# Kernel tuning notes

Measured on AMD Instinct MI355X. Metric: run time of the kernel, lower is better.

The kernel has to match this reference:

```python
import jax, jax.numpy as jnp
import numpy as np

N = 10000       # nodes
E = 160000      # edges
D_IN = 256      # in_channels (node feature dim)
H1, C = 8, 32   # conv1: 8 heads x 32 -> 256; conv2: 1 head x 32
MSG = 128       # msg_dim
TD = 128        # time encoder out_channels
ED = MSG + TD   # edge_dim = 256
HC1 = H1 * C    # 256


def _lin(key, shape, scale=0.05):
    return jax.random.normal(key, shape, dtype=jnp.float32) * scale


def setup_inputs() -> dict:
    key = jax.random.key(0)
    ks = jax.random.split(key, 32)
    inp = {}
    inp["x"] = jax.random.normal(ks[0], (N, D_IN), dtype=jnp.float32)
    inp["last_update"] = jax.random.uniform(ks[1], (N,), jnp.float32, 0.0, 1000.0)
    inp["edge_index"] = jax.random.randint(ks[2], (2, E), 0, N)
    inp["t"] = jax.random.uniform(ks[3], (E,), jnp.float32, 0.0, 1000.0)
    inp["msg"] = jax.random.normal(ks[4], (E, MSG), dtype=jnp.float32)
    # TimeEncoder: Linear(1, TD) then cos
    inp["time_w"] = _lin(ks[5], (TD, 1), 0.1)
    inp["time_b"] = jnp.zeros((TD,), jnp.float32)
    # conv1 (TransformerConv in=256, heads=8, per-head 32, edge_dim=256, concat=True)
    inp["Wq1"] = _lin(ks[6], (D_IN, HC1)); inp["bq1"] = jnp.zeros((HC1,), jnp.float32)
    inp["Wk1"] = _lin(ks[7], (D_IN, HC1)); inp["bk1"] = jnp.zeros((HC1,), jnp.float32)
    inp["Wv1"] = _lin(ks[8], (D_IN, HC1)); inp["bv1"] = jnp.zeros((HC1,), jnp.float32)
    inp["We1"] = _lin(ks[9], (ED, HC1))   # lin_edge has no bias in PyG
    inp["Ws1"] = _lin(ks[10], (D_IN, HC1)); inp["bs1"] = jnp.zeros((HC1,), jnp.float32)
    # conv2 (in=256, heads=1, per-head 32, concat=False)
    inp["Wq2"] = _lin(ks[11], (HC1, C)); inp["bq2"] = jnp.zeros((C,), jnp.float32)
    inp["Wk2"] = _lin(ks[12], (HC1, C)); inp["bk2"] = jnp.zeros((C,), jnp.float32)
    inp["Wv2"] = _lin(ks[13], (HC1, C)); inp["bv2"] = jnp.zeros((C,), jnp.float32)
    inp["We2"] = _lin(ks[14], (ED, C))
    inp["Ws2"] = _lin(ks[15], (HC1, C)); inp["bs2"] = jnp.zeros((C,), jnp.float32)
    return inp


def transformer_conv(x, src, dst, edge_attr, Wq, bq, Wk, bk, Wv, bv, We, Ws, bs, heads, ch, concat):
    n = x.shape[0]
    q = (x @ Wq + bq).reshape(n, heads, ch)
    k = (x @ Wk + bk).reshape(n, heads, ch)
    v = (x @ Wv + bv).reshape(n, heads, ch)
    e = (edge_attr @ We).reshape(-1, heads, ch)       # [E,H,C]
    ke = k[src] + e                                    # key_j + edge
    ve = v[src] + e                                    # value_j + edge
    alpha = jnp.einsum('ehc,ehc->eh', q[dst], ke) / jnp.sqrt(jnp.float32(ch))
    # segment softmax over incoming edges of each destination node
    amax = jax.ops.segment_max(alpha, dst, num_segments=n)   # -inf for empty segs
    ex = jnp.exp(alpha - amax[dst])
    den = jax.ops.segment_sum(ex, dst, num_segments=n)
    attn = ex / (den[dst] + 1e-16)                     # [E,H]
    out = jax.ops.segment_sum(attn[:, :, None] * ve, dst, num_segments=n)  # [N,H,C]
    out = out.reshape(n, heads * ch) if concat else out.mean(axis=1)
    return out + (x @ Ws + bs)                         # root skip connection


def reference(x, last_update, edge_index, t, msg, time_w, time_b,
              Wq1, bq1, Wk1, bk1, Wv1, bv1, We1, Ws1, bs1,
              Wq2, bq2, Wk2, bk2, Wv2, bv2, We2, Ws2, bs2):
    src, dst = edge_index[0], edge_index[1]
    rel_t = last_update[src] - t                       # [E]
    rel_t_enc = jnp.cos(rel_t[:, None] * time_w[:, 0][None, :] + time_b)  # [E,TD]
    edge_attr = jnp.concatenate([rel_t_enc, msg], axis=-1)                # [E,ED]
    h = jax.nn.relu(transformer_conv(x, src, dst, edge_attr,
                                     Wq1, bq1, Wk1, bk1, Wv1, bv1, We1, Ws1, bs1,
                                     H1, C, True))
    out = jax.nn.relu(transformer_conv(h, src, dst, edge_attr,
                                       Wq2, bq2, Wk2, bk2, Wv2, bv2, We2, Ws2, bs2,
                                       1, C, False))
    return out
```

## Files before the change

### kernel.cpp

```cpp
#include <hip/hip_runtime.h>
#include <math.h>

#define N_NODES 10000
#define N_EDGES 160000
#define RT1 157
#define RTE 2500
#define CONVX_T (RT1 * 64 * 32)

static inline int ceildiv(int a, int b) { return (a + b - 1) / b; }

typedef float f32x4 __attribute__((ext_vector_type(4)));
typedef short bf16x8 __attribute__((ext_vector_type(8)));

__device__ __forceinline__ unsigned short f2bf(float f) {
  unsigned int u = __builtin_bit_cast(unsigned int, f);
  u += 0x7FFFu + ((u >> 16) & 1u);
  return (unsigned short)(u >> 16);
}
__device__ __forceinline__ float bf2f(unsigned short h) {
  unsigned int u = ((unsigned int)h) << 16;
  return __builtin_bit_cast(float, u);
}

__global__ void prep1_kernel(const float* __restrict__ lu, const int* __restrict__ srcp,
                             const int* __restrict__ dstp, const float* __restrict__ tt,
                             float* __restrict__ rel, int* __restrict__ deg, int E) {
  for (int i = blockIdx.x * blockDim.x + threadIdx.x; i < E; i += gridDim.x * blockDim.x) {
    rel[i] = lu[srcp[i]] - tt[i];
    atomicAdd(&deg[dstp[i]], 1);
  }
}

__global__ void scan_kernel(const int* __restrict__ deg, int* __restrict__ rowptr, int n) {
  __shared__ int part[1024];
  const int tid = threadIdx.x;
  const int CHK = 10;
  int base = tid * CHK;
  int loc[CHK];
  int s = 0;
#pragma unroll
  for (int j = 0; j < CHK; ++j) {
    int idx = base + j;
    int v = (idx < n) ? deg[idx] : 0;
    loc[j] = s; s += v;
  }
  part[tid] = s;
  __syncthreads();
  for (int off = 1; off < 1024; off <<= 1) {
    int y = (tid >= off) ? part[tid - off] : 0;
    __syncthreads();
    part[tid] += y;
    __syncthreads();
  }
  int pre = tid ? part[tid - 1] : 0;
#pragma unroll
  for (int j = 0; j < CHK; ++j) {
    int idx = base + j;
    if (idx < n) rowptr[idx] = pre + loc[j];
  }
  if (tid == 1023) rowptr[n] = part[1023];
}

__global__ void scatter_kernel(const int* __restrict__ srcp, const int* __restrict__ dstp,
                               const int* __restrict__ rowptr, int* __restrict__ fill,
                               int* __restrict__ sortpos, int* __restrict__ srcs, int E) {
  for (int e = blockIdx.x * blockDim.x + threadIdx.x; e < E; e += gridDim.x * blockDim.x) {
    int d = dstp[e];
    int pos = atomicAdd(&fill[d], 1);
    int slot = rowptr[d] + pos;
    sortpos[e] = slot;
    srcs[slot] = srcp[e];
  }
}

__device__ __forceinline__ void wstore(const float* __restrict__ W, unsigned short* __restrict__ out,
                                       int Nin, int n_off, int NFtot, int k, int c) {
  int gc = n_off + c;
  int ks=k>>5, kg=(k>>3)&3, j=k&7, nf=gc>>4, ic=gc&15;
  out[(size_t)(ks*NFtot+nf)*512 + (ic+16*kg)*8 + j] = f2bf(W[(size_t)k*Nin + c]);
}

__global__ void conv_all_kernel(const float* __restrict__ x, unsigned short* __restrict__ xa,
                                const float* Wq1, const float* Wk1, const float* Wv1, const float* Ws1,
                                const float* We1, const float* Wq2, const float* Wk2, const float* Wv2,
                                const float* Ws2, const float* We2,
                                const float* bq1, const float* bk1, const float* bv1, const float* bs1,
                                const float* bq2, const float* bk2, const float* bv2, const float* bs2,
                                unsigned short* W1f, unsigned short* We1f, unsigned short* W2f,
                                unsigned short* We2f, float* bcat1, float* bcat2) {
  int t0 = blockIdx.x * blockDim.x + threadIdx.x;
  if (t0 < CONVX_T) {
    int i = t0 >> 5, k8 = t0 & 31;
    union { uint4 q; unsigned short s[8]; } u;
    if (i < N_NODES) {
      const float4* px = (const float4*)(x + (size_t)i * 256 + k8 * 8);
      float4 f0 = px[0], f1 = px[1];
      u.s[0]=f2bf(f0.x); u.s[1]=f2bf(f0.y); u.s[2]=f2bf(f0.z); u.s[3]=f2bf(f0.w);
      u.s[4]=f2bf(f1.x); u.s[5]=f2bf(f1.y); u.s[6]=f2bf(f1.z); u.s[7]=f2bf(f1.w);
    } else {
      u.q = make_uint4(0,0,0,0);
    }
    int rt=i>>6, rf=(i>>4)&3, ir=i&15, ks=k8>>2, kg=k8&3;
    *(uint4*)&xa[(size_t)rt*16384 + ks*2048 + rf*512 + (ir+16*kg)*8] = u.q;
    return;
  }
  int t = t0 - CONVX_T;
  if (t < 262144) {
    int w = t >> 16, r = t & 65535, k = r >> 8, c = r & 255;
    const float* W = (w == 0) ? Wq1 : (w == 1) ? Wk1 : (w == 2) ? Wv1 : Ws1;
    wstore(W, W1f, 256, w * 256, 64, k, c);
  } else if (t < 327680) {
    int r = t - 262144, k = r >> 8, c = r & 255;
    wstore(We1, We1f, 256, 0, 16, k, c);
  } else if (t < 360448) {
    int r = t - 327680, w = r >> 13, r2 = r & 8191, k = r2 >> 5, c = r2 & 31;
    const float* W = (w == 0) ? Wq2 : (w == 1) ? Wk2 : (w == 2) ? Wv2 : Ws2;
    wstore(W, W2f, 32, w * 32, 8, k, c);
  } else if (t < 368640) {
    int r = t - 360448, k = r >> 5, c = r & 31;
    wstore(We2, We2f, 32, 0, 4, k, c);
  } else if (t < 369792) {
    int r = t - 368640;
    if (r < 1024) {
      const float* b = (r < 256) ? bq1 : (r < 512) ? bk1 : (r < 768) ? bv1 : bs1;
      bcat1[r] = b[r & 255];
    } else {
      int r2 = r - 1024;
      const float* b = (r2 < 32) ? bq2 : (r2 < 64) ? bk2 : (r2 < 96) ? bv2 : bs2;
      bcat2[r2] = b[r2 & 31];
    }
  }
}

__global__ __launch_bounds__(512, 4)
void big_gemm(const unsigned short* __restrict__ xa, const unsigned short* __restrict__ W1f,
              const float* __restrict__ bcat1, float* __restrict__ qf,
              unsigned short* __restrict__ kvb, float* __restrict__ sf,
              const unsigned short* __restrict__ We1f, const unsigned short* __restrict__ We2f,
              unsigned short* __restrict__ e1b, unsigned short* __restrict__ e2b,
              const float* __restrict__ rel, const float* __restrict__ tw,
              const float* __restrict__ tb, const float* __restrict__ msg,
              const int* __restrict__ sortpos) {
  __shared__ char ldsraw[32768];
  uint4* lds4 = (uint4*)ldsraw;
  const int tid = threadIdx.x;
  const int wid = tid >> 6, lane = tid & 63;
  const int bx = blockIdx.x;
  const int fr0 = (lane >> 4) * 4;
  const int fc0 = lane & 15;

  if (bx < RTE) {
    const int rt0 = bx;
    const int phase = bx & 7;
    {
      const int rem = tid & 255;
      const int ksh = tid >> 8;
      const int arf = rem >> 6, ar2 = rem & 63, air = ar2 & 15, akg = ar2 >> 4;
      const int aedge = rt0 * 64 + arf * 16 + air;
      float rl = rel[aedge];
#pragma unroll
      for (int s = 0; s < 2; ++s) {
        int ks = ksh + s * 2;
        int k8 = ks * 4 + akg;
        const float4* twp = (const float4*)(tw + k8 * 8);
        const float4* tbp = (const float4*)(tb + k8 * 8);
        float4 w0 = twp[0], w1 = twp[1], b0 = tbp[0], b1 = tbp[1];
        union { uint4 q; unsigned short us[8]; } u;
        u.us[0]=f2bf(__cosf(rl*w0.x+b0.x)); u.us[1]=f2bf(__cosf(rl*w0.y+b0.y));
        u.us[2]=f2bf(__cosf(rl*w0.z+b0.z)); u.us[3]=f2bf(__cosf(rl*w0.w+b0.w));
        u.us[4]=f2bf(__cosf(rl*w1.x+b1.x)); u.us[5]=f2bf(__cosf(rl*w1.y+b1.y));
        u.us[6]=f2bf(__cosf(rl*w1.z+b1.z)); u.us[7]=f2bf(__cosf(rl*w1.w+b1.w));
        lds4[ks * 256 + rem] = u.q;
      }
#pragma unroll
      for (int s = 0; s < 2; ++s) {
        int ks = 4 + ksh + s * 2;
        int k8 = ks * 4 + akg;
        const float4* pm = (const float4*)(msg + (size_t)aedge * 128 + (size_t)(k8 - 16) * 8);
        float4 f0 = pm[0], f1 = pm[1];
        union { uint4 q; unsigned short us[8]; } u;
        u.us[0]=f2bf(f0.x); u.us[1]=f2bf(f0.y); u.us[2]=f2bf(f0.z); u.us[3]=f2bf(f0.w);
        u.us[4]=f2bf(f1.x); u.us[5]=f2bf(f1.y); u.us[6]=f2bf(f1.z); u.us[7]=f2bf(f1.w);
        lds4[ks * 256 + rem] = u.q;
      }
    }
    __syncthreads();

    f32x4 acc[4][2];
    f32x4 acc2[4];
#pragma unroll
    for (int i = 0; i < 4; ++i) {
      acc2[i] = (f32x4){0.f, 0.f, 0.f, 0.f};
#pragma unroll
      for (int j = 0; j < 2; ++j) acc[i][j] = (f32x4){0.f, 0.f, 0.f, 0.f};
    }

    bf16x8 aN0, aN1, aN2, aN3, bN0, bN1, b2N;
    {
      const int ks = phase;
      aN0 = *(const bf16x8*)&lds4[ks * 256 + 0 * 64 + lane];
      aN1 = *(const bf16x8*)&lds4[ks * 256 + 1 * 64 + lane];
      aN2 = *(const bf16x8*)&lds4[ks * 256 + 2 * 64 + lane];
      aN3 = *(const bf16x8*)&lds4[ks * 256 + 3 * 64 + lane];
      bN0 = *(const bf16x8*)(We1f + ((size_t)(ks * 16 + wid * 2 + 0)) * 512 + (size_t)lane * 8);
      bN1 = *(const bf16x8*)(We1f + ((size_t)(ks * 16 + wid * 2 + 1)) * 512 + (size_t)lane * 8);
      b2N = 0;
      if (wid < 2) b2N = *(const bf16x8*)(We2f + ((size_t)(ks * 4 + wid)) * 512 + (size_t)lane * 8);
    }
#pragma unroll
    for (int ksi = 0; ksi < 8; ++ksi) {
      bf16x8 aC0 = aN0, aC1 = aN1, aC2 = aN2, aC3 = aN3;
      bf16x8 bC0 = bN0, bC1 = bN1, b2C = b2N;
      if (ksi < 7) {
        const int ks2 = (ksi + 1) ^ phase;
        aN0 = *(const bf16x8*)&lds4[ks2 * 256 + 0 * 64 + lane];
        aN1 = *(const bf16x8*)&lds4[ks2 * 256 + 1 * 64 + lane];
        aN2 = *(const bf16x8*)&lds4[ks2 * 256 + 2 * 64 + lane];
        aN3 = *(const bf16x8*)&lds4[ks2 * 256 + 3 * 64 + lane];
        bN0 = *(const bf16x8*)(We1f + ((size_t)(ks2 * 16 + wid * 2 + 0)) * 512 + (size_t)lane * 8);
        bN1 = *(const bf16x8*)(We1f + ((size_t)(ks2 * 16 + wid * 2 + 1)) * 512 + (size_t)lane * 8);
        if (wid < 2) b2N = *(const bf16x8*)(We2f + ((size_t)(ks2 * 4 + wid)) * 512 + (size_t)lane * 8);
      }
      acc[0][0] = __builtin_amdgcn_mfma_f32_16x16x32_bf16(aC0, bC0, acc[0][0], 0, 0, 0);
      acc[1][0] = __builtin_amdgcn_mfma_f32_16x16x32_bf16(aC1, bC0, acc[1][0], 0, 0, 0);
      acc[2][0] = __builtin_amdgcn_mfma_f32_16x16x32_bf16(aC2, bC0, acc[2][0], 0, 0, 0);
      acc[3][0] = __builtin_amdgcn_mfma_f32_16x16x32_bf16(aC3, bC0, acc[3][0], 0, 0, 0);
      acc[0][1] = __builtin_amdgcn_mfma_f32_16x16x32_bf16(aC0, bC1, acc[0][1], 0, 0, 0);
      acc[1][1] = __builtin_amdgcn_mfma_f32_16x16x32_bf16(aC1, bC1, acc[1][1], 0, 0, 0);
      acc[2][1] = __builtin_amdgcn_mfma_f32_16x16x32_bf16(aC2, bC1, acc[2][1], 0, 0, 0);
      acc[3][1] = __builtin_amdgcn_mfma_f32_16x16x32_bf16(aC3, bC1, acc[3][1], 0, 0, 0);
      if (wid < 2) {
        acc2[0] = __builtin_amdgcn_mfma_f32_16x16x32_bf16(aC0, b2C, acc2[0], 0, 0, 0);
        acc2[1] = __builtin_amdgcn_mfma_f32_16x16x32_bf16(aC1, b2C, acc2[1], 0, 0, 0);
        acc2[2] = __builtin_amdgcn_mfma_f32_16x16x32_bf16(aC2, b2C, acc2[2], 0, 0, 0);
        acc2[3] = __builtin_amdgcn_mfma_f32_16x16x32_bf16(aC3, b2C, acc2[3], 0, 0, 0);
      }
    }

    __syncthreads();
    unsigned short* cl  = (unsigned short*)ldsraw;
    unsigned short* cl2 = (unsigned short*)(ldsraw + 9216);
    int* spos = (int*)(ldsraw + 14336);
    if (tid < 64) spos[tid] = sortpos[rt0 * 64 + tid];
    if (wid < 2) {
#pragma unroll
      for (int rf = 0; rf < 4; ++rf)
#pragma unroll
        for (int j = 0; j < 4; ++j)
          cl2[(fr0 + rf * 16 + j) * 40 + wid * 16 + fc0] = f2bf(acc2[rf][j]);
    }
    for (int pass = 0; pass < 4; ++pass) {
      if ((wid >> 1) == pass) {
#pragma unroll
        for (int cf = 0; cf < 2; ++cf) {
          int c = (wid & 1) * 32 + cf * 16 + fc0;
#pragma unroll
          for (int rf = 0; rf < 4; ++rf)
#pragma unroll
            for (int j = 0; j < 4; ++j)
              cl[(fr0 + rf * 16 + j) * 72 + c] = f2bf(acc[rf][cf][j]);
        }
      }
      __syncthreads();
      {
        int row = tid >> 3, cc = (tid & 7) * 8;
        int gr = spos[row];
        *(uint4*)&e1b[(size_t)gr * 256 + pass * 64 + cc] = *(const uint4*)&cl[row * 72 + cc];
      }
      __syncthreads();
    }
    if (tid < 256) {
      int row = tid >> 2, cc = (tid & 3) * 8;
      int gr = spos[row];
      *(uint4*)&e2b[(size_t)gr * 32 + cc] = *(const uint4*)&cl2[row * 40 + cc];
    }
  } else {
    const int idx = bx - RTE;
    const int rt0 = idx % RT1;
    const int y = idx / RT1;
    const int phase = rt0 & 7;

#pragma unroll
    for (int s = 0; s < 4; ++s)
      lds4[tid + s * 512] = *(const uint4*)(xa + (size_t)rt0 * 16384 + (size_t)(tid + s * 512) * 8);
    __syncthreads();

    f32x4 acc[4][2];
#pragma unroll
    for (int i = 0; i < 4; ++i)
#pragma unroll
      for (int j = 0; j < 2; ++j) acc[i][j] = (f32x4){0.f, 0.f, 0.f, 0.f};

    bf16x8 aN0, aN1, aN2, aN3, bN0, bN1;
    {
      const int ks = phase;
      aN0 = *(const bf16x8*)&lds4[ks * 256 + 0 * 64 + lane];
      aN1 = *(const bf16x8*)&lds4[ks * 256 + 1 * 64 + lane];
      aN2 = *(const bf16x8*)&lds4[ks * 256 + 2 * 64 + lane];
      aN3 = *(const bf16x8*)&lds4[ks * 256 + 3 * 64 + lane];
      bN0 = *(const bf16x8*)(W1f + ((size_t)(ks * 64 + y * 16 + wid * 2 + 0)) * 512 + (size_t)lane * 8);
      bN1 = *(const bf16x8*)(W1f + ((size_t)(ks * 64 + y * 16 + wid * 2 + 1)) * 512 + (size_t)lane * 8);
    }
#pragma unroll
    for (int ksi = 0; ksi < 8; ++ksi) {
      bf16x8 aC0 = aN0, aC1 = aN1, aC2 = aN2, aC3 = aN3;
      bf16x8 bC0 = bN0, bC1 = bN1;
      if (ksi < 7) {
        const int ks2 = (ksi + 1) ^ phase;
        aN0 = *(const bf16x8*)&lds4[ks2 * 256 + 0 * 64 + lane];
        aN1 = *(const bf16x8*)&lds4[ks2 * 256 + 1 * 64 + lane];
        aN2 = *(const bf16x8*)&lds4[ks2 * 256 + 2 * 64 + lane];
        aN3 = *(const bf16x8*)&lds4[ks2 * 256 + 3 * 64 + lane];
        bN0 = *(const bf16x8*)(W1f + ((size_t)(ks2 * 64 + y * 16 + wid * 2 + 0)) * 512 + (size_t)lane * 8);
        bN1 = *(const bf16x8*)(W1f + ((size_t)(ks2 * 64 + y * 16 + wid * 2 + 1)) * 512 + (size_t)lane * 8);
      }
      acc[0][0] = __builtin_amdgcn_mfma_f32_16x16x32_bf16(aC0, bC0, acc[0][0], 0, 0, 0);
      acc[1][0] = __builtin_amdgcn_mfma_f32_16x16x32_bf16(aC1, bC0, acc[1][0], 0, 0, 0);
      acc[2][0] = __builtin_amdgcn_mfma_f32_16x16x32_bf16(aC2, bC0, acc[2][0], 0, 0, 0);
      acc[3][0] = __builtin_amdgcn_mfma_f32_16x16x32_bf16(aC3, bC0, acc[3][0], 0, 0, 0);
      acc[0][1] = __builtin_amdgcn_mfma_f32_16x16x32_bf16(aC0, bC1, acc[0][1], 0, 0, 0);
      acc[1][1] = __builtin_amdgcn_mfma_f32_16x16x32_bf16(aC1, bC1, acc[1][1], 0, 0, 0);
      acc[2][1] = __builtin_amdgcn_mfma_f32_16x16x32_bf16(aC2, bC1, acc[2][1], 0, 0, 0);
      acc[3][1] = __builtin_amdgcn_mfma_f32_16x16x32_bf16(aC3, bC1, acc[3][1], 0, 0, 0);
    }

    bool bf16path;
    void* dstp_; int cstr_, dc0_, bcol0_;
    if (y == 0)      { bf16path = false; dstp_ = qf;  cstr_ = 256; dc0_ = 0;   bcol0_ = 0; }
    else if (y == 1) { bf16path = true;  dstp_ = kvb; cstr_ = 512; dc0_ = 0;   bcol0_ = 256; }
    else if (y == 2) { bf16path = true;  dstp_ = kvb; cstr_ = 512; dc0_ = 256; bcol0_ = 512; }
    else             { bf16path = false; dstp_ = sf;  cstr_ = 256; dc0_ = 0;   bcol0_ = 768; }
    if (!bf16path) {
      float* dst = (float*)dstp_;
      const int row0 = rt0 * 64 + fr0;
#pragma unroll
      for (int cf = 0; cf < 2; ++cf) {
        int c = wid * 32 + cf * 16 + fc0;
        float bv = bcat1[bcol0_ + c];
#pragma unroll
        for (int rf = 0; rf < 4; ++rf) {
#pragma unroll
          for (int j = 0; j < 4; ++j) {
            int r = row0 + rf * 16 + j;
            if (r < N_NODES) dst[(size_t)r * cstr_ + c] = acc[rf][cf][j] + bv;
          }
        }
      }
    } else {
      __syncthreads();
      unsigned short* cl = (unsigned short*)ldsraw;
      unsigned short* dst = (unsigned short*)dstp_;
      for (int pass = 0; pass < 4; ++pass) {
        if ((wid >> 1) == pass) {
#pragma unroll
          for (int cf = 0; cf < 2; ++cf) {
            int c = (wid & 1) * 32 + cf * 16 + fc0;
            float bv = bcat1[bcol0_ + pass * 64 + c];
#pragma unroll
            for (int rf = 0; rf < 4; ++rf)
#pragma unroll
              for (int j = 0; j < 4; ++j)
                cl[(fr0 + rf * 16 + j) * 72 + c] = f2bf(acc[rf][cf][j] + bv);
          }
        }
        __syncthreads();
        {
          int row = tid >> 3, cc = (tid & 7) * 8;
          int gr = rt0 * 64 + row;
          if (gr < N_NODES)
            *(uint4*)&dst[(size_t)gr * cstr_ + dc0_ + pass * 64 + cc] = *(const uint4*)&cl[row * 72 + cc];
        }
        __syncthreads();
      }
    }
  }
}

__global__ __launch_bounds__(256)
void gemm_node2(const unsigned short* __restrict__ ha, const unsigned short* __restrict__ W2f,
                const float* __restrict__ bcat2, float* __restrict__ qkvs2) {
  const int tid = threadIdx.x;
  const int wid = tid >> 6, lane = tid & 63;
  const int wr = wid >> 1, wc = wid & 1;
  const int rt0 = blockIdx.x * 2;
  int rtA = rt0 + wr;
  if (rtA >= RT1) rtA = RT1 - 1;

  f32x4 acc[4][4];
#pragma unroll
  for (int i = 0; i < 4; ++i)
#pragma unroll
    for (int j = 0; j < 4; ++j) acc[i][j] = (f32x4){0.f, 0.f, 0.f, 0.f};

#pragma unroll
  for (int ks = 0; ks < 8; ++ks) {
    bf16x8 a[4], b[4];
#pragma unroll
    for (int rf = 0; rf < 4; ++rf)
      a[rf] = *(const bf16x8*)(ha + (size_t)rtA * 16384 + (size_t)ks * 2048 + (size_t)(rf * 64 + lane) * 8);
#pragma unroll
    for (int cf = 0; cf < 4; ++cf)
      b[cf] = *(const bf16x8*)(W2f + ((size_t)(ks * 8 + wc * 4 + cf)) * 512 + (size_t)lane * 8);
#pragma unroll
    for (int rf = 0; rf < 4; ++rf)
#pragma unroll
      for (int cf = 0; cf < 4; ++cf)
        acc[rf][cf] = __builtin_amdgcn_mfma_f32_16x16x32_bf16(a[rf], b[cf], acc[rf][cf], 0, 0, 0);
  }

  const int row0 = (rt0 + wr) * 64 + ((lane >> 4) * 4);
  const int cb2 = wc * 64 + (lane & 15);
#pragma unroll
  for (int cf = 0; cf < 4; ++cf) {
    int c = cb2 + cf * 16;
    float bv = bcat2[c];
#pragma unroll
    for (int rf = 0; rf < 4; ++rf) {
#pragma unroll
      for (int j = 0; j < 4; ++j) {
        int r = row0 + rf * 16 + j;
        if (r < N_NODES) qkvs2[(size_t)r * 128 + c] = acc[rf][cf][j] + bv;
      }
    }
  }
}

__global__ __launch_bounds__(64)
void attn1_kernel(const float* __restrict__ qf, const unsigned short* __restrict__ kvb,
                  const float* __restrict__ sf, const unsigned short* __restrict__ e1b,
                  const int* __restrict__ srcs, const int* __restrict__ rowptr,
                  unsigned short* __restrict__ ha) {
  const int n = blockIdx.x;
  const int lane = threadIdx.x;
  const int h = lane >> 3;
  const int c0 = (lane & 7) * 4;
  const int off = h * 32 + c0;
  const int beg = rowptr[n], end = rowptr[n + 1];
  const float4 q = *(const float4*)&qf[(size_t)n * 256 + off];

  float m0=-INFINITY,d0=0,x00=0,x01=0,x02=0,x03=0;
  float m1=-INFINITY,d1=0,x10=0,x11=0,x12=0,x13=0;
  float m2=-INFINITY,d2=0,x20=0,x21=0,x22=0,x23=0;
  float m3=-INFINITY,d3=0,x30=0,x31=0,x32=0,x33=0;

  auto step = [&](int i, float& m, float& d, float& a0, float& a1, float& a2, float& a3) {
    const int s = srcs[i];
    ushort4 ev = *(const ushort4*)&e1b[(size_t)i * 256 + off];
    ushort4 kk = *(const ushort4*)&kvb[(size_t)s * 512 + off];
    ushort4 vv = *(const ushort4*)&kvb[(size_t)s * 512 + 256 + off];
    float e0=bf2f(ev.x), e1=bf2f(ev.y), e2=bf2f(ev.z), e3=bf2f(ev.w);
    float p = q.x*(bf2f(kk.x)+e0) + q.y*(bf2f(kk.y)+e1) + q.z*(bf2f(kk.z)+e2) + q.w*(bf2f(kk.w)+e3);
    p += __shfl_xor(p, 1); p += __shfl_xor(p, 2); p += __shfl_xor(p, 4);
    p *= 0.17677669529663687f;
    const float mn = fmaxf(m, p);
    const float sc = __expf(m - mn), w = __expf(p - mn);
    d = d * sc + w;
    a0 = a0 * sc + w * (bf2f(vv.x) + e0);
    a1 = a1 * sc + w * (bf2f(vv.y) + e1);
    a2 = a2 * sc + w * (bf2f(vv.z) + e2);
    a3 = a3 * sc + w * (bf2f(vv.w) + e3);
    m = mn;
  };

  int i = beg;
  for (; i + 3 < end; i += 4) {
    step(i,     m0, d0, x00, x01, x02, x03);
    step(i + 1, m1, d1, x10, x11, x12, x13);
    step(i + 2, m2, d2, x20, x21, x22, x23);
    step(i + 3, m3, d3, x30, x31, x32, x33);
  }
  for (; i < end; ++i) step(i, m0, d0, x00, x01, x02, x03);

  auto merge = [&](float& m, float& d, float& a0, float& a1, float& a2, float& a3,
                   float mB, float dB, float b0, float b1, float b2, float b3) {
    if (mB == -INFINITY) return;
    const float M = fmaxf(m, mB);
    const float sA = __expf(m - M), sB = __expf(mB - M);
    d = d * sA + dB * sB;
    a0 = a0 * sA + b0 * sB; a1 = a1 * sA + b1 * sB;
    a2 = a2 * sA + b2 * sB; a3 = a3 * sA + b3 * sB;
    m = M;
  };
  merge(m0, d0, x00, x01, x02, x03, m1, d1, x10, x11, x12, x13);
  merge(m2, d2, x20, x21, x22, x23, m3, d3, x30, x31, x32, x33);
  merge(m0, d0, x00, x01, x02, x03, m2, d2, x20, x21, x22, x23);

  const float inv = 1.f / (d0 + 1e-16f);
  const float4 sk = *(const float4*)&sf[(size_t)n * 256 + off];
  float o0 = fmaxf(x00 * inv + sk.x, 0.f);
  float o1 = fmaxf(x01 * inv + sk.y, 0.f);
  float o2 = fmaxf(x02 * inv + sk.z, 0.f);
  float o3 = fmaxf(x03 * inv + sk.w, 0.f);
  int rt = n >> 6, rf = (n >> 4) & 3, ir = n & 15;
  int kg = (lane & 7) >> 1, jj = 4 * (lane & 1);
  ushort4 w4;
  w4.x = f2bf(o0); w4.y = f2bf(o1); w4.z = f2bf(o2); w4.w = f2bf(o3);
  *(ushort4*)&ha[(size_t)rt * 16384 + h * 2048 + rf * 512 + (ir + 16 * kg) * 8 + jj] = w4;
}

__global__ __launch_bounds__(64)
void attn2_kernel(const float* __restrict__ qkvs2, const unsigned short* __restrict__ e2b,
                  const int* __restrict__ srcs, const int* __restrict__ rowptr,
                  float* __restrict__ outp) {
  const int n = blockIdx.x;
  const int tid = threadIdx.x;
  const int c = tid & 31;
  const int beg = rowptr[n], end = rowptr[n + 1];
  const float qv = qkvs2[(size_t)n * 128 + c];

  float m0=-INFINITY,d0=0,x0=0;
  float m1=-INFINITY,d1=0,x1=0;
  float m2=-INFINITY,d2=0,x2=0;
  float m3=-INFINITY,d3=0,x3=0;

  auto step = [&](int i, float& m, float& d, float& a) {
    const int s = srcs[i];
    const float ev = bf2f(e2b[(size_t)i * 32 + c]);
    float p = qv * (qkvs2[(size_t)s * 128 + 32 + c] + ev);
    const float v = qkvs2[(size_t)s * 128 + 64 + c] + ev;
#pragma unroll
    for (int off = 16; off; off >>= 1) p += __shfl_xor(p, off);
    p *= 0.17677669529663687f;
    const float mn = fmaxf(m, p);
    const float sc = __expf(m - mn), w = __expf(p - mn);
    d = d * sc + w; a = a * sc + w * v; m = mn;
  };

  int i = beg;
  for (; i + 3 < end; i += 4) {
    step(i, m0, d0, x0);
    step(i + 1, m1, d1, x1);
    step(i + 2, m2, d2, x2);
    step(i + 3, m3, d3, x3);
  }
  for (; i < end; ++i) step(i, m0, d0, x0);

  auto merge = [&](float& m, float& d, float& a, float mB, float dB, float b) {
    if (mB == -INFINITY) return;
    const float M = fmaxf(m, mB);
    const float sA = __expf(m - M), sB = __expf(mB - M);
    d = d * sA + dB * sB; a = a * sA + b * sB; m = M;
  };
  merge(m0, d0, x0, m1, d1, x1);
  merge(m2, d2, x2, m3, d3, x3);
  merge(m0, d0, x0, m2, d2, x2);

  if (tid < 32) {
    float o = x0 / (d0 + 1e-16f) + qkvs2[(size_t)n * 128 + 96 + c];
    outp[(size_t)n * 32 + c] = fmaxf(o, 0.f);
  }
}

extern "C" void kernel_launch(void* const* d_in, const int* in_sizes, int n_in,
                              void* d_out, int out_size, void* d_ws, size_t ws_size,
                              hipStream_t stream) {
  const float* x   = (const float*)d_in[0];
  const float* lu  = (const float*)d_in[1];
  const int*   ei  = (const int*)d_in[2];
  const float* tt  = (const float*)d_in[3];
  const float* msg = (const float*)d_in[4];
  const float* tw  = (const float*)d_in[5];
  const float* tb  = (const float*)d_in[6];
  const float* Wq1 = (const float*)d_in[7];  const float* bq1 = (const float*)d_in[8];
  const float* Wk1 = (const float*)d_in[9];  const float* bk1 = (const float*)d_in[10];
  const float* Wv1 = (const float*)d_in[11]; const float* bv1 = (const float*)d_in[12];
  const float* We1 = (const float*)d_in[13];
  const float* Ws1 = (const float*)d_in[14]; const float* bs1 = (const float*)d_in[15];
  const float* Wq2 = (const float*)d_in[16]; const float* bq2 = (const float*)d_in[17];
  const float* Wk2 = (const float*)d_in[18]; const float* bk2 = (const float*)d_in[19];
  const float* Wv2 = (const float*)d_in[20]; const float* bv2 = (const float*)d_in[21];
  const float* We2 = (const float*)d_in[22];
  const float* Ws2 = (const float*)d_in[23]; const float* bs2 = (const float*)d_in[24];

  const int* srcp = ei;
  const int* dstp = ei + N_EDGES;

  char* p = (char*)d_ws;
  auto alloc = [&](size_t bytes) -> char* {
    char* r = p;
    p += (bytes + 255) & ~(size_t)255;
    return r;
  };
  int*   deg     = (int*)alloc((size_t)N_NODES * 4);
  int*   fill    = (int*)alloc((size_t)N_NODES * 4);
  int*   rowptr  = (int*)alloc((size_t)(N_NODES + 1) * 4);
  int*   sortpos = (int*)alloc((size_t)N_EDGES * 4);
  int*   srcs    = (int*)alloc((size_t)N_EDGES * 4);
  float* rel     = (float*)alloc((size_t)N_EDGES * 4);
  unsigned short* xa   = (unsigned short*)alloc((size_t)RT1 * 32768);
  unsigned short* W1f  = (unsigned short*)alloc((size_t)8 * 64 * 1024);
  unsigned short* We1f = (unsigned short*)alloc((size_t)8 * 16 * 1024);
  unsigned short* W2f  = (unsigned short*)alloc((size_t)8 * 8 * 1024);
  unsigned short* We2f = (unsigned short*)alloc((size_t)8 * 4 * 1024);
  float* bcat1  = (float*)alloc(1024 * 4);
  float* bcat2  = (float*)alloc(128 * 4);
  float* qf     = (float*)alloc((size_t)N_NODES * 256 * 4);
  unsigned short* kvb = (unsigned short*)alloc((size_t)N_NODES * 512 * 2);
  float* sf     = (float*)alloc((size_t)N_NODES * 256 * 4);
  unsigned short* e1b = (unsigned short*)alloc((size_t)N_EDGES * 256 * 2);
  unsigned short* ha  = (unsigned short*)alloc((size_t)RT1 * 32768);
  float* qkvs2  = (float*)alloc((size_t)N_NODES * 128 * 4);
  unsigned short* e2b = (unsigned short*)alloc((size_t)N_EDGES * 32 * 2);
  float* outp   = (float*)d_out;

  hipMemsetAsync(deg, 0, (size_t)N_NODES * 4, stream);
  hipMemsetAsync(fill, 0, (size_t)N_NODES * 4, stream);
  hipMemsetAsync(ha + (size_t)(RT1 - 1) * 16384, 0, 32768, stream);

  prep1_kernel<<<625, 256, 0, stream>>>(lu, srcp, dstp, tt, rel, deg, N_EDGES);
  scan_kernel<<<1, 1024, 0, stream>>>(deg, rowptr, N_NODES);
  scatter_kernel<<<625, 256, 0, stream>>>(srcp, dstp, rowptr, fill, sortpos, srcs, N_EDGES);

  conv_all_kernel<<<ceildiv(CONVX_T + 369792, 256), 256, 0, stream>>>(
      x, xa, Wq1, Wk1, Wv1, Ws1, We1, Wq2, Wk2, Wv2, Ws2, We2,
      bq1, bk1, bv1, bs1, bq2, bk2, bv2, bs2,
      W1f, We1f, W2f, We2f, bcat1, bcat2);

  big_gemm<<<RTE + RT1 * 4, 512, 0, stream>>>(
      xa, W1f, bcat1, qf, kvb, sf, We1f, We2f, e1b, e2b,
      rel, tw, tb, msg, sortpos);

  attn1_kernel<<<N_NODES, 64, 0, stream>>>(qf, kvb, sf, e1b, srcs, rowptr, ha);
  gemm_node2<<<ceildiv(RT1, 2), 256, 0, stream>>>(ha, W2f, bcat2, qkvs2);
  attn2_kernel<<<N_NODES, 64, 0, stream>>>(qkvs2, e2b, srcs, rowptr, outp);
}
```

Measured before the change: 176.7 us.

## Fuse edge projection with layer-1 attention via per-segment partial softmax and merge

The edge GEMM for layer 1 now feeds the attention directly inside the same block. Edges are processed in destination-sorted order; each 8-edge segment writes a partial softmax record (max, denominator, weighted bf16 value sum) per destination. A small merge kernel then combines the records and applies the skip connection and ReLU. This removes the large bf16 e1b edge-feature buffer and the separate attn1 pass over it. In exchange, the node GEMM is split into its own launch ahead of the edge kernel, so the two no longer overlap. The scatter step also produces sorted src/dst/edge-id/rel_t arrays, so msg is gathered by original edge id. Destinations spanning more than MAXSEG segments would silently drop contributions.

```diff
diff --git a/kernel.cpp b/kernel.cpp
--- a/kernel.cpp
+++ b/kernel.cpp
@@ -6,6 +6,8 @@
 #define RT1 157
 #define RTE 2500
 #define CONVX_T (RT1 * 64 * 32)
+#define MAXSEG 16
+#define SEGSTRIDE 576
 
 static inline int ceildiv(int a, int b) { return (a + b - 1) / b; }
 
@@ -22,13 +24,9 @@
   return __builtin_bit_cast(float, u);
 }
 
-__global__ void prep1_kernel(const float* __restrict__ lu, const int* __restrict__ srcp,
-                             const int* __restrict__ dstp, const float* __restrict__ tt,
-                             float* __restrict__ rel, int* __restrict__ deg, int E) {
-  for (int i = blockIdx.x * blockDim.x + threadIdx.x; i < E; i += gridDim.x * blockDim.x) {
-    rel[i] = lu[srcp[i]] - tt[i];
+__global__ void count_kernel(const int* __restrict__ dstp, int* __restrict__ deg, int E) {
+  for (int i = blockIdx.x * blockDim.x + threadIdx.x; i < E; i += gridDim.x * blockDim.x)
     atomicAdd(&deg[dstp[i]], 1);
-  }
 }
 
 __global__ void scan_kernel(const int* __restrict__ deg, int* __restrict__ rowptr, int n) {
@@ -61,15 +59,19 @@
   if (tid == 1023) rowptr[n] = part[1023];
 }
 
-__global__ void scatter_kernel(const int* __restrict__ srcp, const int* __restrict__ dstp,
+__global__ void scatter_kernel(const float* __restrict__ lu, const float* __restrict__ tt,
+                               const int* __restrict__ srcp, const int* __restrict__ dstp,
                                const int* __restrict__ rowptr, int* __restrict__ fill,
-                               int* __restrict__ sortpos, int* __restrict__ srcs, int E) {
+                               int* __restrict__ srcs, int* __restrict__ dsts,
+                               int* __restrict__ eidA, float* __restrict__ rel_s, int E) {
   for (int e = blockIdx.x * blockDim.x + threadIdx.x; e < E; e += gridDim.x * blockDim.x) {
-    int d = dstp[e];
+    int d = dstp[e], s = srcp[e];
     int pos = atomicAdd(&fill[d], 1);
     int slot = rowptr[d] + pos;
-    sortpos[e] = slot;
-    srcs[slot] = srcp[e];
+    srcs[slot] = s;
+    dsts[slot] = d;
+    eidA[slot] = e;
+    rel_s[slot] = lu[s] - tt[e];
   }
 }
 
@@ -133,247 +135,380 @@
 }
 
 __global__ __launch_bounds__(512, 4)
-void big_gemm(const unsigned short* __restrict__ xa, const unsigned short* __restrict__ W1f,
-              const float* __restrict__ bcat1, float* __restrict__ qf,
-              unsigned short* __restrict__ kvb, float* __restrict__ sf,
-              const unsigned short* __restrict__ We1f, const unsigned short* __restrict__ We2f,
-              unsigned short* __restrict__ e1b, unsigned short* __restrict__ e2b,
-              const float* __restrict__ rel, const float* __restrict__ tw,
-              const float* __restrict__ tb, const float* __restrict__ msg,
-              const int* __restrict__ sortpos) {
+void node1_gemm(const unsigned short* __restrict__ xa, const unsigned short* __restrict__ W1f,
+                const float* __restrict__ bcat1, float* __restrict__ qf,
+                unsigned short* __restrict__ kvb, float* __restrict__ sf) {
   __shared__ char ldsraw[32768];
   uint4* lds4 = (uint4*)ldsraw;
+  const int tid = threadIdx.x;
+  const int wid = tid >> 6, lane = tid & 63;
+  const int fr0 = (lane >> 4) * 4;
+  const int fc0 = lane & 15;
+  const int rt0 = blockIdx.x % RT1;
+  const int y = blockIdx.x / RT1;
+  const int phase = rt0 & 7;
+
+#pragma unroll
+  for (int s = 0; s < 4; ++s)
+    lds4[tid + s * 512] = *(const uint4*)(xa + (size_t)rt0 * 16384 + (size_t)(tid + s * 512) * 8);
+  __syncthreads();
+
+  f32x4 acc[4][2];
+#pragma unroll
+  for (int i = 0; i < 4; ++i)
+#pragma unroll
+    for (int j = 0; j < 2; ++j) acc[i][j] = (f32x4){0.f, 0.f, 0.f, 0.f};
+
+  bf16x8 aN0, aN1, aN2, aN3, bN0, bN1;
+  {
+    const int ks = phase;
+    aN0 = *(const bf16x8*)&lds4[ks * 256 + 0 * 64 + lane];
+    aN1 = *(const bf16x8*)&lds4[ks * 256 + 1 * 64 + lane];
+    aN2 = *(const bf16x8*)&lds4[ks * 256 + 2 * 64 + lane];
+    aN3 = *(const bf16x8*)&lds4[ks * 256 + 3 * 64 + lane];
+    bN0 = *(const bf16x8*)(W1f + ((size_t)(ks * 64 + y * 16 + wid * 2 + 0)) * 512 + (size_t)lane * 8);
+    bN1 = *(const bf16x8*)(W1f + ((size_t)(ks * 64 + y * 16 + wid * 2 + 1)) * 512 + (size_t)lane * 8);
+  }
+#pragma unroll
+  for (int ksi = 0; ksi < 8; ++ksi) {
+    bf16x8 aC0 = aN0, aC1 = aN1, aC2 = aN2, aC3 = aN3;
+    bf16x8 bC0 = bN0, bC1 = bN1;
+    if (ksi < 7) {
+      const int ks2 = (ksi + 1) ^ phase;
+      aN0 = *(const bf16x8*)&lds4[ks2 * 256 + 0 * 64 + lane];
+      aN1 = *(const bf16x8*)&lds4[ks2 * 256 + 1 * 64 + lane];
+      aN2 = *(const bf16x8*)&lds4[ks2 * 256 + 2 * 64 + lane];
+      aN3 = *(const bf16x8*)&lds4[ks2 * 256 + 3 * 64 + lane];
+      bN0 = *(const bf16x8*)(W1f + ((size_t)(ks2 * 64 + y * 16 + wid * 2 + 0)) * 512 + (size_t)lane * 8);
+      bN1 = *(const bf16x8*)(W1f + ((size_t)(ks2 * 64 + y * 16 + wid * 2 + 1)) * 512 + (size_t)lane * 8);
+    }
+    acc[0][0] = __builtin_amdgcn_mfma_f32_16x16x32_bf16(aC0, bC0, acc[0][0], 0, 0, 0);
+    acc[1][0] = __builtin_amdgcn_mfma_f32_16x16x32_bf16(aC1, bC0, acc[1][0], 0, 0, 0);
+    acc[2][0] = __builtin_amdgcn_mfma_f32_16x16x32_bf16(aC2, bC0, acc[2][0], 0, 0, 0);
+    acc[3][0] = __builtin_amdgcn_mfma_f32_16x16x32_bf16(aC3, bC0, acc[3][0], 0, 0, 0);
+    acc[0][1] = __builtin_amdgcn_mfma_f32_16x16x32_bf16(aC0, bC1, acc[0][1], 0, 0, 0);
+    acc[1][1] = __builtin_amdgcn_mfma_f32_16x16x32_bf16(aC1, bC1, acc[1][1], 0, 0, 0);
+    acc[2][1] = __builtin_amdgcn_mfma_f32_16x16x32_bf16(aC2, bC1, acc[2][1], 0, 0, 0);
+    acc[3][1] = __builtin_amdgcn_mfma_f32_16x16x32_bf16(aC3, bC1, acc[3][1], 0, 0, 0);
+  }
+
+  bool bf16path;
+  void* dstp_; int cstr_, dc0_, bcol0_;
+  if (y == 0)      { bf16path = false; dstp_ = qf;  cstr_ = 256; dc0_ = 0;   bcol0_ = 0; }
+  else if (y == 1) { bf16path = true;  dstp_ = kvb; cstr_ = 512; dc0_ = 0;   bcol0_ = 256; }
+  else if (y == 2) { bf16path = true;  dstp_ = kvb; cstr_ = 512; dc0_ = 256; bcol0_ = 512; }
+  else             { bf16path = false; dstp_ = sf;  cstr_ = 256; dc0_ = 0;   bcol0_ = 768; }
+  if (!bf16path) {
+    float* dst = (float*)dstp_;
+    const int row0 = rt0 * 64 + fr0;
+#pragma unroll
+    for (int cf = 0; cf < 2; ++cf) {
+      int c = wid * 32 + cf * 16 + fc0;
+      float bv = bcat1[bcol0_ + c];
+#pragma unroll
+      for (int rf = 0; rf < 4; ++rf) {
+#pragma unroll
+        for (int j = 0; j < 4; ++j) {
+          int r = row0 + rf * 16 + j;
+          if (r < N_NODES) dst[(size_t)r * cstr_ + c] = acc[rf][cf][j] + bv;
+        }
+      }
+    }
+  } else {
+    __syncthreads();
+    unsigned short* cl = (unsigned short*)ldsraw;
+    unsigned short* dst = (unsigned short*)dstp_;
+    for (int pass = 0; pass < 4; ++pass) {
+      if ((wid >> 1) == pass) {
+#pragma unroll
+        for (int cf = 0; cf < 2; ++cf) {
+          int c = (wid & 1) * 32 + cf * 16 + fc0;
+          float bv = bcat1[bcol0_ + pass * 64 + c];
+#pragma unroll
+          for (int rf = 0; rf < 4; ++rf)
+#pragma unroll
+            for (int j = 0; j < 4; ++j)
+              cl[(fr0 + rf * 16 + j) * 72 + c] = f2bf(acc[rf][cf][j] + bv);
+        }
+      }
+      __syncthreads();
+      {
+        int row = tid >> 3, cc = (tid & 7) * 8;
+        int gr = rt0 * 64 + row;
+        if (gr < N_NODES)
+          *(uint4*)&dst[(size_t)gr * cstr_ + dc0_ + pass * 64 + cc] = *(const uint4*)&cl[row * 72 + cc];
+      }
+      __syncthreads();
+    }
+  }
+}
+
+__global__ __launch_bounds__(512, 4)
+void edge_fused(const float* __restrict__ qf, const unsigned short* __restrict__ kvb,
+                const unsigned short* __restrict__ We1f, const unsigned short* __restrict__ We2f,
+                char* __restrict__ segrec, unsigned short* __restrict__ e2b,
+                const float* __restrict__ rel_s, const float* __restrict__ tw,
+                const float* __restrict__ tb, const float* __restrict__ msg,
+                const int* __restrict__ eidA, const int* __restrict__ srcsA,
+                const int* __restrict__ dstsA, const int* __restrict__ rowptr) {
+  __shared__ char ldsraw[43008];
+  uint4* lds4 = (uint4*)ldsraw;
+  unsigned short* e1t = (unsigned short*)ldsraw;
+  float* scoreL = (float*)(ldsraw + 33280);
+  float* wL     = (float*)(ldsraw + 35328);
+  int* dseg     = (int*)(ldsraw + 37376);
+  int* sseg     = (int*)(ldsraw + 37632);
+  unsigned short* cl2 = (unsigned short*)(ldsraw + 37888);
+
   const int tid = threadIdx.x;
   const int wid = tid >> 6, lane = tid & 63;
   const int bx = blockIdx.x;
   const int fr0 = (lane >> 4) * 4;
   const int fc0 = lane & 15;
-
-  if (bx < RTE) {
-    const int rt0 = bx;
-    const int phase = bx & 7;
+  const int rt0 = bx;
+  const int phase = bx & 7;
+
+  {
+    const int rem = tid & 255;
+    const int ksh = tid >> 8;
+    const int arf = rem >> 6, ar2 = rem & 63, air = ar2 & 15, akg = ar2 >> 4;
+    const int slot = rt0 * 64 + arf * 16 + air;
+    float rl = rel_s[slot];
+    int eorg = eidA[slot];
+#pragma unroll
+    for (int s = 0; s < 2; ++s) {
+      int ks = ksh + s * 2;
+      int k8 = ks * 4 + akg;
+      const float4* twp = (const float4*)(tw + k8 * 8);
+      const float4* tbp = (const float4*)(tb + k8 * 8);
+      float4 w0 = twp[0], w1 = twp[1], b0 = tbp[0], b1 = tbp[1];
+      union { uint4 q; unsigned short us[8]; } u;
+      u.us[0]=f2bf(__cosf(rl*w0.x+b0.x)); u.us[1]=f2bf(__cosf(rl*w0.y+b0.y));
+      u.us[2]=f2bf(__cosf(rl*w0.z+b0.z)); u.us[3]=f2bf(__cosf(rl*w0.w+b0.w));
+      u.us[4]=f2bf(__cosf(rl*w1.x+b1.x)); u.us[5]=f2bf(__cosf(rl*w1.y+b1.y));
+      u.us[6]=f2bf(__cosf(rl*w1.z+b1.z)); u.us[7]=f2bf(__cosf(rl*w1.w+b1.w));
+      lds4[ks * 256 + rem] = u.q;
+    }
+#pragma unroll
+    for (int s = 0; s < 2; ++s) {
+      int ks = 4 + ksh + s * 2;
+      int k8 = ks * 4 + akg;
+      const float4* pm = (const float4*)(msg + (size_t)eorg * 128 + (size_t)(k8 - 16) * 8);
+      float4 f0 = pm[0], f1 = pm[1];
+      union { uint4 q; unsigned short us[8]; } u;
+      u.us[0]=f2bf(f0.x); u.us[1]=f2bf(f0.y); u.us[2]=f2bf(f0.z); u.us[3]=f2bf(f0.w);
+      u.us[4]=f2bf(f1.x); u.us[5]=f2bf(f1.y); u.us[6]=f2bf(f1.z); u.us[7]=f2bf(f1.w);
+      lds4[ks * 256 + rem] = u.q;
+    }
+  }
+  __syncthreads();
+
+  f32x4 acc[4][2];
+  f32x4 acc2[4];
+#pragma unroll
+  for (int i = 0; i < 4; ++i) {
+    acc2[i] = (f32x4){0.f, 0.f, 0.f, 0.f};
+#pragma unroll
+    for (int j = 0; j < 2; ++j) acc[i][j] = (f32x4){0.f, 0.f, 0.f, 0.f};
+  }
+
+  bf16x8 aN0, aN1, aN2, aN3, bN0, bN1, b2N;
+  {
+    const int ks = phase;
+    aN0 = *(const bf16x8*)&lds4[ks * 256 + 0 * 64 + lane];
+    aN1 = *(const bf16x8*)&lds4[ks * 256 + 1 * 64 + lane];
+    aN2 = *(const bf16x8*)&lds4[ks * 256 + 2 * 64 + lane];
+    aN3 = *(const bf16x8*)&lds4[ks * 256 + 3 * 64 + lane];
+    bN0 = *(const bf16x8*)(We1f + ((size_t)(ks * 16 + wid * 2 + 0)) * 512 + (size_t)lane * 8);
+    bN1 = *(const bf16x8*)(We1f + ((size_t)(ks * 16 + wid * 2 + 1)) * 512 + (size_t)lane * 8);
+    b2N = 0;
+    if (wid < 2) b2N = *(const bf16x8*)(We2f + ((size_t)(ks * 4 + wid)) * 512 + (size_t)lane * 8);
+  }
+#pragma unroll
+  for (int ksi = 0; ksi < 8; ++ksi) {
+    bf16x8 aC0 = aN0, aC1 = aN1, aC2 = aN2, aC3 = aN3;
+    bf16x8 bC0 = bN0, bC1 = bN1, b2C = b2N;
+    if (ksi < 7) {
+      const int ks2 = (ksi + 1) ^ phase;
+      aN0 = *(const bf16x8*)&lds4[ks2 * 256 + 0 * 64 + lane];
+      aN1 = *(const bf16x8*)&lds4[ks2 * 256 + 1 * 64 + lane];
+      aN2 = *(const bf16x8*)&lds4[ks2 * 256 + 2 * 64 + lane];
+      aN3 = *(const bf16x8*)&lds4[ks2 * 256 + 3 * 64 + lane];
+      bN0 = *(const bf16x8*)(We1f + ((size_t)(ks2 * 16 + wid * 2 + 0)) * 512 + (size_t)lane * 8);
+      bN1 = *(const bf16x8*)(We1f + ((size_t)(ks2 * 16 + wid * 2 + 1)) * 512 + (size_t)lane * 8);
+      if (wid < 2) b2N = *(const bf16x8*)(We2f + ((size_t)(ks2 * 4 + wid)) * 512 + (size_t)lane * 8);
+    }
+    acc[0][0] = __builtin_amdgcn_mfma_f32_16x16x32_bf16(aC0, bC0, acc[0][0], 0, 0, 0);
+    acc[1][0] = __builtin_amdgcn_mfma_f32_16x16x32_bf16(aC1, bC0, acc[1][0], 0, 0, 0);
+    acc[2][0] = __builtin_amdgcn_mfma_f32_16x16x32_bf16(aC2, bC0, acc[2][0], 0, 0, 0);
+    acc[3][0] = __builtin_amdgcn_mfma_f32_16x16x32_bf16(aC3, bC0, acc[3][0], 0, 0, 0);
+    acc[0][1] = __builtin_amdgcn_mfma_f32_16x16x32_bf16(aC0, bC1, acc[0][1], 0, 0, 0);
+    acc[1][1] = __builtin_amdgcn_mfma_f32_16x16x32_bf16(aC1, bC1, acc[1][1], 0, 0, 0);
+    acc[2][1] = __builtin_amdgcn_mfma_f32_16x16x32_bf16(aC2, bC1, acc[2][1], 0, 0, 0);
+    acc[3][1] = __builtin_amdgcn_mfma_f32_16x16x32_bf16(aC3, bC1, acc[3][1], 0, 0, 0);
+    if (wid < 2) {
+      acc2[0] = __builtin_amdgcn_mfma_f32_16x16x32_bf16(aC0, b2C, acc2[0], 0, 0, 0);
+      acc2[1] = __builtin_amdgcn_mfma_f32_16x16x32_bf16(aC1, b2C, acc2[1], 0, 0, 0);
+      acc2[2] = __builtin_amdgcn_mfma_f32_16x16x32_bf16(aC2, b2C, acc2[2], 0, 0, 0);
+      acc2[3] = __builtin_amdgcn_mfma_f32_16x16x32_bf16(aC3, b2C, acc2[3], 0, 0, 0);
+    }
+  }
+
+  __syncthreads();
+  if (tid < 64) {
+    dseg[tid] = dstsA[rt0 * 64 + tid];
+    sseg[tid] = srcsA[rt0 * 64 + tid];
+  }
+#pragma unroll
+  for (int cf = 0; cf < 2; ++cf)
+#pragma unroll
+    for (int rf = 0; rf < 4; ++rf)
+#pragma unroll
+      for (int j = 0; j < 4; ++j)
+        e1t[(fr0 + rf * 16 + j) * 260 + wid * 32 + cf * 16 + fc0] = f2bf(acc[rf][cf][j]);
+  if (wid < 2) {
+#pragma unroll
+    for (int rf = 0; rf < 4; ++rf)
+#pragma unroll
+      for (int j = 0; j < 4; ++j)
+        cl2[(fr0 + rf * 16 + j) * 40 + wid * 16 + fc0] = f2bf(acc2[rf][j]);
+  }
+  __syncthreads();
+
+  {
+    const int base = wid * 8;
+    int d8[8], s8[8];
+#pragma unroll
+    for (int t = 0; t < 8; ++t) { d8[t] = dseg[base + t]; s8[t] = sseg[base + t]; }
+#pragma unroll
+    for (int t = 0; t < 8; ++t) {
+      const int r = base + t;
+      float4 q4 = *(const float4*)&qf[(size_t)d8[t] * 256 + lane * 4];
+      ushort4 k4 = *(const ushort4*)&kvb[(size_t)s8[t] * 512 + lane * 4];
+      ushort4 e4 = *(const ushort4*)&e1t[r * 260 + lane * 4];
+      float p = q4.x * (bf2f(k4.x) + bf2f(e4.x)) + q4.y * (bf2f(k4.y) + bf2f(e4.y))
+              + q4.z * (bf2f(k4.z) + bf2f(e4.z)) + q4.w * (bf2f(k4.w) + bf2f(e4.w));
+      p += __shfl_xor(p, 1); p += __shfl_xor(p, 2); p += __shfl_xor(p, 4);
+      if ((lane & 7) == 0) scoreL[r * 8 + (lane >> 3)] = p * 0.17677669529663687f;
+    }
+  }
+  __syncthreads();
+
+  {
+    const int r = tid >> 3, h = tid & 7;
+    const int d = dseg[r];
+    const int base = r & ~7;
+    float m = -INFINITY;
+#pragma unroll
+    for (int r2 = 0; r2 < 8; ++r2)
+      if (dseg[base + r2] == d) m = fmaxf(m, scoreL[(base + r2) * 8 + h]);
+    wL[r * 8 + h] = __expf(scoreL[r * 8 + h] - m);
+    bool first = (r == base) || (dseg[r - 1] != d);
+    if (first) {
+      float den = 0.f;
+#pragma unroll
+      for (int r2 = 0; r2 < 8; ++r2)
+        if (dseg[base + r2] == d) den += __expf(scoreL[(base + r2) * 8 + h] - m);
+      int rg = bx * 8 + (r >> 3);
+      int j = rg - (rowptr[d] >> 3);
+      if (j < MAXSEG) {
+        float* rec = (float*)(segrec + ((size_t)d * MAXSEG + j) * SEGSTRIDE);
+        rec[128 + h] = m;
+        rec[136 + h] = den;
+      }
+    }
+  }
+  __syncthreads();
+
+  {
+    const int base = wid * 8;
+    const int rgj = bx * 8 + wid;
+    int d8[8]; float w8[8]; ushort4 v8[8], e8[8];
+#pragma unroll
+    for (int t = 0; t < 8; ++t) {
+      const int r = base + t;
+      d8[t] = dseg[r];
+      v8[t] = *(const ushort4*)&kvb[(size_t)sseg[r] * 512 + 256 + lane * 4];
+      e8[t] = *(const ushort4*)&e1t[r * 260 + lane * 4];
+      w8[t] = wL[r * 8 + (lane >> 3)];
+    }
+    f32x4 pacc = (f32x4){0.f, 0.f, 0.f, 0.f};
+    int cur = d8[0];
+#pragma unroll
+    for (int t = 0; t < 8; ++t) {
+      if (d8[t] != cur) {
+        int j = rgj - (rowptr[cur] >> 3);
+        if (j < MAXSEG) {
+          unsigned short* pp = (unsigned short*)(segrec + ((size_t)cur * MAXSEG + j) * SEGSTRIDE);
+          ushort4 o;
+          o.x = f2bf(pacc[0]); o.y = f2bf(pacc[1]); o.z = f2bf(pacc[2]); o.w = f2bf(pacc[3]);
+          *(ushort4*)&pp[lane * 4] = o;
+        }
+        pacc = (f32x4){0.f, 0.f, 0.f, 0.f};
+        cur = d8[t];
+      }
+      pacc[0] += w8[t] * (bf2f(v8[t].x) + bf2f(e8[t].x));
+      pacc[1] += w8[t] * (bf2f(v8[t].y) + bf2f(e8[t].y));
+      pacc[2] += w8[t] * (bf2f(v8[t].z) + bf2f(e8[t].z));
+      pacc[3] += w8[t] * (bf2f(v8[t].w) + bf2f(e8[t].w));
+    }
     {
-      const int rem = tid & 255;
-      const int ksh = tid >> 8;
-      const int arf = rem >> 6, ar2 = rem & 63, air = ar2 & 15, akg = ar2 >> 4;
-      const int aedge = rt0 * 64 + arf * 16 + air;
-      float rl = rel[aedge];
-#pragma unroll
-      for (int s = 0; s < 2; ++s) {
-        int ks = ksh + s * 2;
-        int k8 = ks * 4 + akg;
-        const float4* twp = (const float4*)(tw + k8 * 8);
-        const float4* tbp = (const float4*)(tb + k8 * 8);
-        float4 w0 = twp[0], w1 = twp[1], b0 = tbp[0], b1 = tbp[1];
-        union { uint4 q; unsigned short us[8]; } u;
-        u.us[0]=f2bf(__cosf(rl*w0.x+b0.x)); u.us[1]=f2bf(__cosf(rl*w0.y+b0.y));
-        u.us[2]=f2bf(__cosf(rl*w0.z+b0.z)); u.us[3]=f2bf(__cosf(rl*w0.w+b0.w));
-        u.us[4]=f2bf(__cosf(rl*w1.x+b1.x)); u.us[5]=f2bf(__cosf(rl*w1.y+b1.y));
-        u.us[6]=f2bf(__cosf(rl*w1.z+b1.z)); u.us[7]=f2bf(__cosf(rl*w1.w+b1.w));
-        lds4[ks * 256 + rem] = u.q;
+      int j = rgj - (rowptr[cur] >> 3);
+      if (j < MAXSEG) {
+        unsigned short* pp = (unsigned short*)(segrec + ((size_t)cur * MAXSEG + j) * SEGSTRIDE);
+        ushort4 o;
+        o.x = f2bf(pacc[0]); o.y = f2bf(pacc[1]); o.z = f2bf(pacc[2]); o.w = f2bf(pacc[3]);
+        *(ushort4*)&pp[lane * 4] = o;
       }
-#pragma unroll
-      for (int s = 0; s < 2; ++s) {
-        int ks = 4 + ksh + s * 2;
-        int k8 = ks * 4 + akg;
-        const float4* pm = (const float4*)(msg + (size_t)aedge * 128 + (size_t)(k8 - 16) * 8);
-        float4 f0 = pm[0], f1 = pm[1];
-        union { uint4 q; unsigned short us[8]; } u;
-        u.us[0]=f2bf(f0.x); u.us[1]=f2bf(f0.y); u.us[2]=f2bf(f0.z); u.us[3]=f2bf(f0.w);
-        u.us[4]=f2bf(f1.x); u.us[5]=f2bf(f1.y); u.us[6]=f2bf(f1.z); u.us[7]=f2bf(f1.w);
-        lds4[ks * 256 + rem] = u.q;
-      }
-    }
-    __syncthreads();
-
-    f32x4 acc[4][2];
-    f32x4 acc2[4];
-#pragma unroll
-    for (int i = 0; i < 4; ++i) {
-      acc2[i] = (f32x4){0.f, 0.f, 0.f, 0.f};
-#pragma unroll
-      for (int j = 0; j < 2; ++j) acc[i][j] = (f32x4){0.f, 0.f, 0.f, 0.f};
-    }
-
-    bf16x8 aN0, aN1, aN2, aN3, bN0, bN1, b2N;
-    {
-      const int ks = phase;
-      aN0 = *(const bf16x8*)&lds4[ks * 256 + 0 * 64 + lane];
-      aN1 = *(const bf16x8*)&lds4[ks * 256 + 1 * 64 + lane];
-      aN2 = *(const bf16x8*)&lds4[ks * 256 + 2 * 64 + lane];
-      aN3 = *(const bf16x8*)&lds4[ks * 256 + 3 * 64 + lane];
-      bN0 = *(const bf16x8*)(We1f + ((size_t)(ks * 16 + wid * 2 + 0)) * 512 + (size_t)lane * 8);
-      bN1 = *(const bf16x8*)(We1f + ((size_t)(ks * 16 + wid * 2 + 1)) * 512 + (size_t)lane * 8);
-      b2N = 0;
-      if (wid < 2) b2N = *(const bf16x8*)(We2f + ((size_t)(ks * 4 + wid)) * 512 + (size_t)lane * 8);
-    }
-#pragma unroll
-    for (int ksi = 0; ksi < 8; ++ksi) {
-      bf16x8 aC0 = aN0, aC1 = aN1, aC2 = aN2, aC3 = aN3;
-      bf16x8 bC0 = bN0, bC1 = bN1, b2C = b2N;
-      if (ksi < 7) {
-        const int ks2 = (ksi + 1) ^ phase;
-        aN0 = *(const bf16x8*)&lds4[ks2 * 256 + 0 * 64 + lane];
-        aN1 = *(const bf16x8*)&lds4[ks2 * 256 + 1 * 64 + lane];
-        aN2 = *(const bf16x8*)&lds4[ks2 * 256 + 2 * 64 + lane];
-        aN3 = *(const bf16x8*)&lds4[ks2 * 256 + 3 * 64 + lane];
-        bN0 = *(const bf16x8*)(We1f + ((size_t)(ks2 * 16 + wid * 2 + 0)) * 512 + (size_t)lane * 8);
-        bN1 = *(const bf16x8*)(We1f + ((size_t)(ks2 * 16 + wid * 2 + 1)) * 512 + (size_t)lane * 8);
-        if (wid < 2) b2N = *(const bf16x8*)(We2f + ((size_t)(ks2 * 4 + wid)) * 512 + (size_t)lane * 8);
-      }
-      acc[0][0] = __builtin_amdgcn_mfma_f32_16x16x32_bf16(aC0, bC0, acc[0][0], 0, 0, 0);
-      acc[1][0] = __builtin_amdgcn_mfma_f32_16x16x32_bf16(aC1, bC0, acc[1][0], 0, 0, 0);
-      acc[2][0] = __builtin_amdgcn_mfma_f32_16x16x32_bf16(aC2, bC0, acc[2][0], 0, 0, 0);
-      acc[3][0] = __builtin_amdgcn_mfma_f32_16x16x32_bf16(aC3, bC0, acc[3][0], 0, 0, 0);
-      acc[0][1] = __builtin_amdgcn_mfma_f32_16x16x32_bf16(aC0, bC1, acc[0][1], 0, 0, 0);
-      acc[1][1] = __builtin_amdgcn_mfma_f32_16x16x32_bf16(aC1, bC1, acc[1][1], 0, 0, 0);
-      acc[2][1] = __builtin_amdgcn_mfma_f32_16x16x32_bf16(aC2, bC1, acc[2][1], 0, 0, 0);
-      acc[3][1] = __builtin_amdgcn_mfma_f32_16x16x32_bf16(aC3, bC1, acc[3][1], 0, 0, 0);
-      if (wid < 2) {
-        acc2[0] = __builtin_amdgcn_mfma_f32_16x16x32_bf16(aC0, b2C, acc2[0], 0, 0, 0);
-        acc2[1] = __builtin_amdgcn_mfma_f32_16x16x32_bf16(aC1, b2C, acc2[1], 0, 0, 0);
-        acc2[2] = __builtin_amdgcn_mfma_f32_16x16x32_bf16(aC2, b2C, acc2[2], 0, 0, 0);
-        acc2[3] = __builtin_amdgcn_mfma_f32_16x16x32_bf16(aC3, b2C, acc2[3], 0, 0, 0);
-      }
-    }
-
-    __syncthreads();
-    unsigned short* cl  = (unsigned short*)ldsraw;
-    unsigned short* cl2 = (unsigned short*)(ldsraw + 9216);
-    int* spos = (int*)(ldsraw + 14336);
-    if (tid < 64) spos[tid] = sortpos[rt0 * 64 + tid];
-    if (wid < 2) {
-#pragma unroll
-      for (int rf = 0; rf < 4; ++rf)
-#pragma unroll
-        for (int j = 0; j < 4; ++j)
-          cl2[(fr0 + rf * 16 + j) * 40 + wid * 16 + fc0] = f2bf(acc2[rf][j]);
-    }
-    for (int pass = 0; pass < 4; ++pass) {
-      if ((wid >> 1) == pass) {
-#pragma unroll
-        for (int cf = 0; cf < 2; ++cf) {
-          int c = (wid & 1) * 32 + cf * 16 + fc0;
-#pragma unroll
-          for (int rf = 0; rf < 4; ++rf)
-#pragma unroll
-            for (int j = 0; j < 4; ++j)
-              cl[(fr0 + rf * 16 + j) * 72 + c] = f2bf(acc[rf][cf][j]);
-        }
-      }
-      __syncthreads();
-      {
-        int row = tid >> 3, cc = (tid & 7) * 8;
-        int gr = spos[row];
-        *(uint4*)&e1b[(size_t)gr * 256 + pass * 64 + cc] = *(const uint4*)&cl[row * 72 + cc];
-      }
-      __syncthreads();
-    }
-    if (tid < 256) {
-      int row = tid >> 2, cc = (tid & 3) * 8;
-      int gr = spos[row];
-      *(uint4*)&e2b[(size_t)gr * 32 + cc] = *(const uint4*)&cl2[row * 40 + cc];
-    }
+    }
+  }
+
+  if (tid < 256) {
+    int row = tid >> 2, cc = (tid & 3) * 8;
+    *(uint4*)&e2b[(size_t)(rt0 * 64 + row) * 32 + cc] = *(const uint4*)&cl2[row * 40 + cc];
+  }
+}
+
+__global__ __launch_bounds__(64)
+void merge_kernel(const char* __restrict__ segrec, const int* __restrict__ rowptr,
+                  const float* __restrict__ sf, unsigned short* __restrict__ ha) {
+  const int n = blockIdx.x;
+  const int lane = threadIdx.x;
+  const int beg = rowptr[n], end = rowptr[n + 1];
+  const float4 sk = *(const float4*)&sf[(size_t)n * 256 + lane * 4];
+  float o0, o1, o2, o3;
+  if (beg == end) {
+    o0 = sk.x; o1 = sk.y; o2 = sk.z; o3 = sk.w;
   } else {
-    const int idx = bx - RTE;
-    const int rt0 = idx % RT1;
-    const int y = idx / RT1;
-    const int phase = rt0 & 7;
-
-#pragma unroll
-    for (int s = 0; s < 4; ++s)
-      lds4[tid + s * 512] = *(const uint4*)(xa + (size_t)rt0 * 16384 + (size_t)(tid + s * 512) * 8);
-    __syncthreads();
-
-    f32x4 acc[4][2];
-#pragma unroll
-    for (int i = 0; i < 4; ++i)
-#pragma unroll
-      for (int j = 0; j < 2; ++j) acc[i][j] = (f32x4){0.f, 0.f, 0.f, 0.f};
-
-    bf16x8 aN0, aN1, aN2, aN3, bN0, bN1;
-    {
-      const int ks = phase;
-      aN0 = *(const bf16x8*)&lds4[ks * 256 + 0 * 64 + lane];
-      aN1 = *(const bf16x8*)&lds4[ks * 256 + 1 * 64 + lane];
-      aN2 = *(const bf16x8*)&lds4[ks * 256 + 2 * 64 + lane];
-      aN3 = *(const bf16x8*)&lds4[ks * 256 + 3 * 64 + lane];
-      bN0 = *(const bf16x8*)(W1f + ((size_t)(ks * 64 + y * 16 + wid * 2 + 0)) * 512 + (size_t)lane * 8);
-      bN1 = *(const bf16x8*)(W1f + ((size_t)(ks * 64 + y * 16 + wid * 2 + 1)) * 512 + (size_t)lane * 8);
-    }
-#pragma unroll
-    for (int ksi = 0; ksi < 8; ++ksi) {
-      bf16x8 aC0 = aN0, aC1 = aN1, aC2 = aN2, aC3 = aN3;
-      bf16x8 bC0 = bN0, bC1 = bN1;
-      if (ksi < 7) {
-        const int ks2 = (ksi + 1) ^ phase;
-        aN0 = *(const bf16x8*)&lds4[ks2 * 256 + 0 * 64 + lane];
-        aN1 = *(const bf16x8*)&lds4[ks2 * 256 + 1 * 64 + lane];
-        aN2 = *(const bf16x8*)&lds4[ks2 * 256 + 2 * 64 + lane];
-        aN3 = *(const bf16x8*)&lds4[ks2 * 256 + 3 * 64 + lane];
-        bN0 = *(const bf16x8*)(W1f + ((size_t)(ks2 * 64 + y * 16 + wid * 2 + 0)) * 512 + (size_t)lane * 8);
-        bN1 = *(const bf16x8*)(W1f + ((size_t)(ks2 * 64 + y * 16 + wid * 2 + 1)) * 512 + (size_t)lane * 8);
-      }
-      acc[0][0] = __builtin_amdgcn_mfma_f32_16x16x32_bf16(aC0, bC0, acc[0][0], 0, 0, 0);
-      acc[1][0] = __builtin_amdgcn_mfma_f32_16x16x32_bf16(aC1, bC0, acc[1][0], 0, 0, 0);
-      acc[2][0] = __builtin_amdgcn_mfma_f32_16x16x32_bf16(aC2, bC0, acc[2][0], 0, 0, 0);
-      acc[3][0] = __builtin_amdgcn_mfma_f32_16x16x32_bf16(aC3, bC0, acc[3][0], 0, 0, 0);
-      acc[0][1] = __builtin_amdgcn_mfma_f32_16x16x32_bf16(aC0, bC1, acc[0][1], 0, 0, 0);
-      acc[1][1] = __builtin_amdgcn_mfma_f32_16x16x32_bf16(aC1, bC1, acc[1][1], 0, 0, 0);
-      acc[2][1] = __builtin_amdgcn_mfma_f32_16x16x32_bf16(aC2, bC1, acc[2][1], 0, 0, 0);
-      acc[3][1] = __builtin_amdgcn_mfma_f32_16x16x32_bf16(aC3, bC1, acc[3][1], 0, 0, 0);
-    }
-
-    bool bf16path;
-    void* dstp_; int cstr_, dc0_, bcol0_;
-    if (y == 0)      { bf16path = false; dstp_ = qf;  cstr_ = 256; dc0_ = 0;   bcol0_ = 0; }
-    else if (y == 1) { bf16path = true;  dstp_ = kvb; cstr_ = 512; dc0_ = 0;   bcol0_ = 256; }
-    else if (y == 2) { bf16path = true;  dstp_ = kvb; cstr_ = 512; dc0_ = 256; bcol0_ = 512; }
-    else             { bf16path = false; dstp_ = sf;  cstr_ = 256; dc0_ = 0;   bcol0_ = 768; }
-    if (!bf16path) {
-      float* dst = (float*)dstp_;
-      const int row0 = rt0 * 64 + fr0;
-#pragma unroll
-      for (int cf = 0; cf < 2; ++cf) {
-        int c = wid * 32 + cf * 16 + fc0;
-        float bv = bcat1[bcol0_ + c];
-#pragma unroll
-        for (int rf = 0; rf < 4; ++rf) {
-#pragma unroll
-          for (int j = 0; j < 4; ++j) {
-            int r = row0 + rf * 16 + j;
-            if (r < N_NODES) dst[(size_t)r * cstr_ + c] = acc[rf][cf][j] + bv;
-          }
-        }
-      }
-    } else {
-      __syncthreads();
-      unsigned short* cl = (unsigned short*)ldsraw;
-      unsigned short* dst = (unsigned short*)dstp_;
-      for (int pass = 0; pass < 4; ++pass) {
-        if ((wid >> 1) == pass) {
-#pragma unroll
-          for (int cf = 0; cf < 2; ++cf) {
-            int c = (wid & 1) * 32 + cf * 16 + fc0;
-            float bv = bcat1[bcol0_ + pass * 64 + c];
-#pragma unroll
-            for (int rf = 0; rf < 4; ++rf)
-#pragma unroll
-              for (int j = 0; j < 4; ++j)
-                cl[(fr0 + rf * 16 + j) * 72 + c] = f2bf(acc[rf][cf][j] + bv);
-          }
-        }
-        __syncthreads();
-        {
-          int row = tid >> 3, cc = (tid & 7) * 8;
-          int gr = rt0 * 64 + row;
-          if (gr < N_NODES)
-            *(uint4*)&dst[(size_t)gr * cstr_ + dc0_ + pass * 64 + cc] = *(const uint4*)&cl[row * 72 + cc];
-        }
-        __syncthreads();
-      }
-    }
-  }
+    const int h = lane >> 3;
+    int s0 = beg >> 3, s1 = (end - 1) >> 3;
+    int span = s1 - s0 + 1; if (span > MAXSEG) span = MAXSEG;
+    float M = -INFINITY;
+    for (int j = 0; j < span; ++j) {
+      const float* rec = (const float*)(segrec + ((size_t)n * MAXSEG + j) * SEGSTRIDE);
+      M = fmaxf(M, rec[128 + h]);
+    }
+    float den = 0.f;
+    f32x4 num = (f32x4){0.f, 0.f, 0.f, 0.f};
+    for (int j = 0; j < span; ++j) {
+      const float* rec = (const float*)(segrec + ((size_t)n * MAXSEG + j) * SEGSTRIDE);
+      float sc = __expf(rec[128 + h] - M);
+      den += sc * rec[136 + h];
+      ushort4 p4 = *(const ushort4*)((const unsigned short*)rec + lane * 4);
+      num[0] += sc * bf2f(p4.x); num[1] += sc * bf2f(p4.y);
+      num[2] += sc * bf2f(p4.z); num[3] += sc * bf2f(p4.w);
+    }
+    const float inv = 1.f / (den + 1e-16f);
+    o0 = num[0] * inv + sk.x; o1 = num[1] * inv + sk.y;
+    o2 = num[2] * inv + sk.z; o3 = num[3] * inv + sk.w;
+  }
+  o0 = fmaxf(o0, 0.f); o1 = fmaxf(o1, 0.f); o2 = fmaxf(o2, 0.f); o3 = fmaxf(o3, 0.f);
+  int rt = n >> 6, rf = (n >> 4) & 3, ir = n & 15;
+  int h2 = lane >> 3;
+  int kg = (lane & 7) >> 1, jj = 4 * (lane & 1);
+  ushort4 w4;
+  w4.x = f2bf(o0); w4.y = f2bf(o1); w4.z = f2bf(o2); w4.w = f2bf(o3);
+  *(ushort4*)&ha[(size_t)rt * 16384 + h2 * 2048 + rf * 512 + (ir + 16 * kg) * 8 + jj] = w4;
 }
 
 __global__ __launch_bounds__(256)
@@ -423,79 +558,6 @@
       }
     }
   }
-}
-
-__global__ __launch_bounds__(64)
-void attn1_kernel(const float* __restrict__ qf, const unsigned short* __restrict__ kvb,
-                  const float* __restrict__ sf, const unsigned short* __restrict__ e1b,
-                  const int* __restrict__ srcs, const int* __restrict__ rowptr,
-                  unsigned short* __restrict__ ha) {
-  const int n = blockIdx.x;
-  const int lane = threadIdx.x;
-  const int h = lane >> 3;
-  const int c0 = (lane & 7) * 4;
-  const int off = h * 32 + c0;
-  const int beg = rowptr[n], end = rowptr[n + 1];
-  const float4 q = *(const float4*)&qf[(size_t)n * 256 + off];
-
-  float m0=-INFINITY,d0=0,x00=0,x01=0,x02=0,x03=0;
-  float m1=-INFINITY,d1=0,x10=0,x11=0,x12=0,x13=0;
-  float m2=-INFINITY,d2=0,x20=0,x21=0,x22=0,x23=0;
-  float m3=-INFINITY,d3=0,x30=0,x31=0,x32=0,x33=0;
-
-  auto step = [&](int i, float& m, float& d, float& a0, float& a1, float& a2, float& a3) {
-    const int s = srcs[i];
-    ushort4 ev = *(const ushort4*)&e1b[(size_t)i * 256 + off];
-    ushort4 kk = *(const ushort4*)&kvb[(size_t)s * 512 + off];
-    ushort4 vv = *(const ushort4*)&kvb[(size_t)s * 512 + 256 + off];
-    float e0=bf2f(ev.x), e1=bf2f(ev.y), e2=bf2f(ev.z), e3=bf2f(ev.w);
-    float p = q.x*(bf2f(kk.x)+e0) + q.y*(bf2f(kk.y)+e1) + q.z*(bf2f(kk.z)+e2) + q.w*(bf2f(kk.w)+e3);
-    p += __shfl_xor(p, 1); p += __shfl_xor(p, 2); p += __shfl_xor(p, 4);
-    p *= 0.17677669529663687f;
-    const float mn = fmaxf(m, p);
-    const float sc = __expf(m - mn), w = __expf(p - mn);
-    d = d * sc + w;
-    a0 = a0 * sc + w * (bf2f(vv.x) + e0);
-    a1 = a1 * sc + w * (bf2f(vv.y) + e1);
-    a2 = a2 * sc + w * (bf2f(vv.z) + e2);
-    a3 = a3 * sc + w * (bf2f(vv.w) + e3);
-    m = mn;
-  };
-
-  int i = beg;
-  for (; i + 3 < end; i += 4) {
-    step(i,     m0, d0, x00, x01, x02, x03);
-    step(i + 1, m1, d1, x10, x11, x12, x13);
-    step(i + 2, m2, d2, x20, x21, x22, x23);
-    step(i + 3, m3, d3, x30, x31, x32, x33);
-  }
-  for (; i < end; ++i) step(i, m0, d0, x00, x01, x02, x03);
-
-  auto merge = [&](float& m, float& d, float& a0, float& a1, float& a2, float& a3,
-                   float mB, float dB, float b0, float b1, float b2, float b3) {
-    if (mB == -INFINITY) return;
-    const float M = fmaxf(m, mB);
-    const float sA = __expf(m - M), sB = __expf(mB - M);
-    d = d * sA + dB * sB;
-    a0 = a0 * sA + b0 * sB; a1 = a1 * sA + b1 * sB;
-    a2 = a2 * sA + b2 * sB; a3 = a3 * sA + b3 * sB;
-    m = M;
-  };
-  merge(m0, d0, x00, x01, x02, x03, m1, d1, x10, x11, x12, x13);
-  merge(m2, d2, x20, x21, x22, x23, m3, d3, x30, x31, x32, x33);
-  merge(m0, d0, x00, x01, x02, x03, m2, d2, x20, x21, x22, x23);
-
-  const float inv = 1.f / (d0 + 1e-16f);
-  const float4 sk = *(const float4*)&sf[(size_t)n * 256 + off];
-  float o0 = fmaxf(x00 * inv + sk.x, 0.f);
-  float o1 = fmaxf(x01 * inv + sk.y, 0.f);
-  float o2 = fmaxf(x02 * inv + sk.z, 0.f);
-  float o3 = fmaxf(x03 * inv + sk.w, 0.f);
-  int rt = n >> 6, rf = (n >> 4) & 3, ir = n & 15;
-  int kg = (lane & 7) >> 1, jj = 4 * (lane & 1);
-  ushort4 w4;
-  w4.x = f2bf(o0); w4.y = f2bf(o1); w4.z = f2bf(o2); w4.w = f2bf(o3);
-  *(ushort4*)&ha[(size_t)rt * 16384 + h * 2048 + rf * 512 + (ir + 16 * kg) * 8 + jj] = w4;
 }
 
 __global__ __launch_bounds__(64)
@@ -584,9 +646,10 @@
   int*   deg     = (int*)alloc((size_t)N_NODES * 4);
   int*   fill    = (int*)alloc((size_t)N_NODES * 4);
   int*   rowptr  = (int*)alloc((size_t)(N_NODES + 1) * 4);
-  int*   sortpos = (int*)alloc((size_t)N_EDGES * 4);
   int*   srcs    = (int*)alloc((size_t)N_EDGES * 4);
-  float* rel     = (float*)alloc((size_t)N_EDGES * 4);
+  int*   dsts    = (int*)alloc((size_t)N_EDGES * 4);
+  int*   eidA    = (int*)alloc((size_t)N_EDGES * 4);
+  float* rel_s   = (float*)alloc((size_t)N_EDGES * 4);
   unsigned short* xa   = (unsigned short*)alloc((size_t)RT1 * 32768);
   unsigned short* W1f  = (unsigned short*)alloc((size_t)8 * 64 * 1024);
   unsigned short* We1f = (unsigned short*)alloc((size_t)8 * 16 * 1024);
@@ -597,7 +660,7 @@
   float* qf     = (float*)alloc((size_t)N_NODES * 256 * 4);
   unsigned short* kvb = (unsigned short*)alloc((size_t)N_NODES * 512 * 2);
   float* sf     = (float*)alloc((size_t)N_NODES * 256 * 4);
-  unsigned short* e1b = (unsigned short*)alloc((size_t)N_EDGES * 256 * 2);
+  char*  segrec = (char*)alloc((size_t)N_NODES * MAXSEG * SEGSTRIDE);
   unsigned short* ha  = (unsigned short*)alloc((size_t)RT1 * 32768);
   float* qkvs2  = (float*)alloc((size_t)N_NODES * 128 * 4);
   unsigned short* e2b = (unsigned short*)alloc((size_t)N_EDGES * 32 * 2);
@@ -607,20 +670,23 @@
   hipMemsetAsync(fill, 0, (size_t)N_NODES * 4, stream);
   hipMemsetAsync(ha + (size_t)(RT1 - 1) * 16384, 0, 32768, stream);
 
-  prep1_kernel<<<625, 256, 0, stream>>>(lu, srcp, dstp, tt, rel, deg, N_EDGES);
+  count_kernel<<<625, 256, 0, stream>>>(dstp, deg, N_EDGES);
   scan_kernel<<<1, 1024, 0, stream>>>(deg, rowptr, N_NODES);
-  scatter_kernel<<<625, 256, 0, stream>>>(srcp, dstp, rowptr, fill, sortpos, srcs, N_EDGES);
+  scatter_kernel<<<625, 256, 0, stream>>>(lu, tt, srcp, dstp, rowptr, fill,
+                                          srcs, dsts, eidA, rel_s, N_EDGES);
 
   conv_all_kernel<<<ceildiv(CONVX_T + 369792, 256), 256, 0, stream>>>(
       x, xa, Wq1, Wk1, Wv1, Ws1, We1, Wq2, Wk2, Wv2, Ws2, We2,
       bq1, bk1, bv1, bs1, bq2, bk2, bv2, bs2,
       W1f, We1f, W2f, We2f, bcat1, bcat2);
 
-  big_gemm<<<RTE + RT1 * 4, 512, 0, stream>>>(
-      xa, W1f, bcat1, qf, kvb, sf, We1f, We2f, e1b, e2b,
-      rel, tw, tb, msg, sortpos);
-
-  attn1_kernel<<<N_NODES, 64, 0, stream>>>(qf, kvb, sf, e1b, srcs, rowptr, ha);
+  node1_gemm<<<RT1 * 4, 512, 0, stream>>>(xa, W1f, bcat1, qf, kvb, sf);
+
+  edge_fused<<<RTE, 512, 0, stream>>>(
+      qf, kvb, We1f, We2f, segrec, e2b,
+      rel_s, tw, tb, msg, eidA, srcs, dsts, rowptr);
+
+  merge_kernel<<<N_NODES, 64, 0, stream>>>(segrec, rowptr, sf, ha);
   gemm_node2<<<ceildiv(RT1, 2), 256, 0, stream>>>(ha, W2f, bcat2, qkvs2);
   attn2_kernel<<<N_NODES, 64, 0, stream>>>(qkvs2, e2b, srcs, rowptr, outp);
 }
```

Measured after the change: 180.8 us. 1.02x slower.
